# Performance work log

Measured on AMD Instinct MI355X. Metric: run time of the kernel, lower is better.

Reference implementation:

```python
import jax, jax.numpy as jnp
import numpy as np

KH, KW = 3, 3
SH, SW = 1, 1
IC, OC = 32, 32
M = 4
P = M * M
ITERS = 3
LAM = 1.0
EPS = 1e-8


def _patches(t, kh, kw, sh, sw):
    # t: [B, H, W, ...] -> [B, Ho, Wo, kh, kw, ...] (im2col, matches torch unfold+permute)
    H, W = t.shape[1], t.shape[2]
    Ho = (H - kh) // sh + 1
    Wo = (W - kw) // sw + 1
    i = (jnp.arange(Ho) * sh)[:, None] + jnp.arange(kh)[None, :]  # [Ho,kh]
    j = (jnp.arange(Wo) * sw)[:, None] + jnp.arange(kw)[None, :]  # [Wo,kw]
    tp = t[:, i]            # [B,Ho,kh,W,...]
    tp = tp[:, :, :, j]     # [B,Ho,kh,Wo,kw,...]
    return jnp.moveaxis(tp, 2, 3)  # [B,Ho,Wo,kh,kw,...]


def setup_inputs() -> dict:
    key = jax.random.key(0)
    k1, k2, k3, k4, k5 = jax.random.split(key, 5)
    x = jax.random.normal(k1, (4, 14, 14, IC, M, M), dtype=jnp.float32)
    a = jax.random.uniform(k2, (4, 14, 14, IC), dtype=jnp.float32)
    W = jax.random.uniform(k3, (KH, KW, IC, OC, M, M), dtype=jnp.float32)   # torch.rand init
    beta_u = jax.random.uniform(k4, (1, OC, 1), dtype=jnp.float32)
    beta_a = jax.random.uniform(k5, (1, OC), dtype=jnp.float32)
    return {"x": x, "a": a, "W": W, "beta_u": beta_u, "beta_a": beta_a}


def reference(x, a, W, beta_u, beta_a):
    # im2col patches
    xp = _patches(x, KH, KW, SH, SW)          # [B,Ho,Wo,kh,kw,IC,M,M]
    ap = _patches(a, KH, KW, SH, SW)          # [B,Ho,Wo,kh,kw,IC]
    # pose-transform votes: per (kh,kw,inCap,outCap) 4x4 matmul
    V = jnp.einsum('bhwklcxy,klcoyz->bhwklcoxz', xp, W)
    B, Ho, Wo = V.shape[:3]
    N = KH * KW * IC
    V = V.reshape(B, Ho, Wo, N, OC, P)        # votes
    a_in = ap.reshape(B, Ho, Wo, N)
    bu = beta_u.reshape(OC, 1)
    ba = beta_a.reshape(OC)

    # EM routing (Hinton et al. 2018, fixed inverse temperature)
    R = jnp.full((B, Ho, Wo, N, OC), 1.0 / OC, dtype=V.dtype)
    for it in range(ITERS):
        Ra = R * a_in[..., None]                                  # [B,Ho,Wo,N,OC]
        Rs = Ra.sum(axis=3) + EPS                                 # [B,Ho,Wo,OC]
        mu = jnp.einsum('bhwno,bhwnop->bhwop', Ra, V) / Rs[..., None]
        d = V - mu[:, :, :, None]                                 # [B,Ho,Wo,N,OC,P]
        sig2 = jnp.einsum('bhwno,bhwnop->bhwop', Ra, d * d) / Rs[..., None] + EPS
        cost = (bu + 0.5 * jnp.log(sig2)) * Rs[..., None]         # [B,Ho,Wo,OC,P]
        a_out = jax.nn.sigmoid(LAM * (ba - cost.sum(-1)))         # [B,Ho,Wo,OC]
        if it < ITERS - 1:
            logp = -0.5 * jnp.sum(d * d / sig2[:, :, :, None] + jnp.log(sig2)[:, :, :, None], axis=-1)
            R = jax.nn.softmax(jnp.log(a_out + EPS)[:, :, :, None] + logp, axis=-1)

    pose = mu.reshape(B, Ho, Wo, OC, M, M)
    return pose, a_out
```

## Files before the change

### kernel.cpp

```cpp
#include <hip/hip_runtime.h>


#define EPSV 1e-8f

template <int CTRL>
__device__ __forceinline__ float dppf(float v) {
  return __int_as_float(__builtin_amdgcn_update_dpp(
      0, __float_as_int(v), CTRL, 0xf, 0xf, true));
}
__device__ __forceinline__ float swz16(float v) {
  return __int_as_float(__builtin_amdgcn_ds_swizzle(__float_as_int(v), 0x401F));
}
__device__ __forceinline__ float red_max32(float v) {
  v = fmaxf(v, dppf<0xB1>(v));
  v = fmaxf(v, dppf<0x4E>(v));
  v = fmaxf(v, dppf<0x141>(v));
  v = fmaxf(v, dppf<0x140>(v));
  v = fmaxf(v, swz16(v));
  return v;
}
__device__ __forceinline__ float red_sum32(float v) {
  v += dppf<0xB1>(v);
  v += dppf<0x4E>(v);
  v += dppf<0x141>(v);
  v += dppf<0x140>(v);
  v += swz16(v);
  return v;
}

__device__ __forceinline__ void compute_votes(const float* __restrict__ Wt,
                                              const float* __restrict__ xr,
                                              int n, int o, float* __restrict__ V)
{
  float Wf[16];
  {
    const float* wp = Wt + (((n << 5) + o) << 4);
#pragma unroll
    for (int i = 0; i < 4; ++i) {
      const float4 q = *(const float4*)(wp + (i << 2));
      Wf[i*4+0]=q.x; Wf[i*4+1]=q.y; Wf[i*4+2]=q.z; Wf[i*4+3]=q.w;
    }
  }
  float xv[16];
#pragma unroll
  for (int i = 0; i < 4; ++i) {
    const float4 q = *(const float4*)(xr + (i << 2));
    xv[i*4+0]=q.x; xv[i*4+1]=q.y; xv[i*4+2]=q.z; xv[i*4+3]=q.w;
  }
#pragma unroll
  for (int xi = 0; xi < 4; ++xi)
#pragma unroll
    for (int z = 0; z < 4; ++z)
      V[xi*4+z] = fmaf(xv[xi*4+0], Wf[z],
                  fmaf(xv[xi*4+1], Wf[4+z],
                  fmaf(xv[xi*4+2], Wf[8+z],
                       xv[xi*4+3]* Wf[12+z])));
}

__global__ __launch_bounds__(512, 4) void caps_stats(
    const float* __restrict__ X, const float* __restrict__ A, const float* __restrict__ Wt,
    const float* __restrict__ Bu, const float* __restrict__ Ba,
    const float* __restrict__ prev, float* __restrict__ cur, int it)
{
  __shared__ float xp_s[144*16];
  __shared__ float a_s[144];
  __shared__ float part[8*544];
  __shared__ float prs[8*32];
  __shared__ float mu_t[512], isig_t[512], lsig_t[512];
  __shared__ float la_s[32], slog_s[32], rs_s[32];

  const int t    = threadIdx.x;
  const int o    = t & 31;
  const int ng   = t >> 5;
  const int wv   = t >> 6;
  const int lane = t & 63;

  const int bid  = blockIdx.x;
  const int pos  = bid >> 1;
  const int half = bid & 1;
  const int b  = pos / 144;
  const int r_ = pos - b*144;
  const int h  = r_ / 12;
  const int w  = r_ - (r_/12)*12;
  const int nbase = half * 144;

  for (int i = t; i < 576; i += 512) {
    const int r  = i >> 2, q4 = i & 3;
    const int n  = nbase + r;
    const int kl = n >> 5, c = n & 31;
    const int hy = h + kl/3, wx = w + (kl - (kl/3)*3);
    const float4 v = *(const float4*)(X + ((((b*14+hy)*14+wx) << 9) + (c << 4) + (q4 << 2)));
    *(float4*)(xp_s + (r << 4) + (q4 << 2)) = v;
  }
  if (t < 144) {
    const int n  = nbase + t;
    const int kl = n >> 5, c = n & 31;
    const int hy = h + kl/3, wx = w + (kl - (kl/3)*3);
    a_s[t] = A[((b*14+hy)*14+wx)*32 + c];
  }

  float mu_r[16], isig_r[16];
  float la_r = 0.f, slog_r = 0.f;

  if (it > 0) {
    {
      const int pi = t >> 5, oo = t & 31;
      const float* h0 = prev + (pos*2+0)*1056;
      const float* h1 = prev + (pos*2+1)*1056;
      const int idx = pi*32 + oo;
      const float s1   = h0[idx]       + h1[idx];
      const float s2   = h0[512+idx]   + h1[512+idx];
      const float rsum = h0[1024+oo]   + h1[1024+oo] + EPSV;
      const float mu = s1 / rsum;
      float var = s2 / rsum - mu*mu;
      var = fmaxf(var, 0.f);
      const float sg = var + EPSV;
      mu_t[idx]   = mu;
      isig_t[idx] = 1.0f / sg;
      lsig_t[idx] = __logf(sg);
      if (pi == 0) rs_s[oo] = rsum;
    }
    __syncthreads();
    if (t < 32) {
      float slog = 0.f;
#pragma unroll
      for (int p = 0; p < 16; ++p) slog += lsig_t[p*32 + t];
      const float cost = rs_s[t] * (16.0f*Bu[t] + 0.5f*slog);
      const float av = 1.0f / (1.0f + __expf(-(Ba[t] - cost)));
      la_s[t]   = __logf(av + EPSV);
      slog_s[t] = slog;
    }
    __syncthreads();
#pragma unroll
    for (int p = 0; p < 16; ++p) { mu_r[p] = mu_t[p*32 + o]; isig_r[p] = isig_t[p*32 + o]; }
    slog_r = slog_s[o];
    la_r   = la_s[o];
  } else {
#pragma unroll
    for (int p = 0; p < 16; ++p) { mu_r[p] = 0.f; isig_r[p] = 0.f; }
    __syncthreads();
  }

  float S1[16], S2[16];
#pragma unroll
  for (int p = 0; p < 16; ++p) { S1[p] = 0.f; S2[p] = 0.f; }
  float rs = 0.f;

#pragma unroll 1
  for (int j = 0; j < 9; ++j) {
    const int nl = ng + (j << 4);
    const int n  = nbase + nl;
    float V[16];
    compute_votes(Wt, xp_s + (nl << 4), n, o, V);

    float ra;
    if (it == 0) {
      ra = a_s[nl] * (1.0f/32.0f);
    } else {
      float q0 = 0.f, q1 = 0.f, q2 = 0.f, q3 = 0.f;
#pragma unroll
      for (int p = 0; p < 4; ++p) {
        float d;
        d = V[p]    - mu_r[p];    q0 = fmaf(d*d, isig_r[p],    q0);
        d = V[p+4]  - mu_r[p+4];  q1 = fmaf(d*d, isig_r[p+4],  q1);
        d = V[p+8]  - mu_r[p+8];  q2 = fmaf(d*d, isig_r[p+8],  q2);
        d = V[p+12] - mu_r[p+12]; q3 = fmaf(d*d, isig_r[p+12], q3);
      }
      const float q = slog_r + ((q0 + q1) + (q2 + q3));
      const float z = la_r - 0.5f*q;
      const float m  = red_max32(z);
      const float ev = __expf(z - m);
      const float s  = red_sum32(ev);
      ra = (ev / s) * a_s[nl];
    }
    rs += ra;
#pragma unroll
    for (int p = 0; p < 16; ++p) {
      const float rv = ra * V[p];
      S1[p] += rv;
      S2[p] = fmaf(rv, V[p], S2[p]);
    }
  }

#pragma unroll
  for (int p = 0; p < 16; ++p) {
    S1[p] += __shfl_xor(S1[p], 32);
    S2[p] += __shfl_xor(S2[p], 32);
  }
  rs += __shfl_xor(rs, 32);

  float* dst = cur + bid*1056;

  if (lane < 32) {
    float* p1 = part + wv*544 + o*17;
#pragma unroll
    for (int p = 0; p < 16; ++p) p1[p] = S1[p];
    prs[wv*32 + o] = rs;
  }
  __syncthreads();
  {
    const int pi = t >> 5, oo = t & 31;
    float s1 = 0.f;
#pragma unroll
    for (int g = 0; g < 8; ++g) s1 += part[g*544 + oo*17 + pi];
    dst[t] = s1;
    if (t < 32) {
      float r = 0.f;
#pragma unroll
      for (int g = 0; g < 8; ++g) r += prs[(g << 5) + t];
      dst[1024 + t] = r;
    }
  }
  __syncthreads();

  if (lane < 32) {
    float* p2 = part + wv*544 + o*17;
#pragma unroll
    for (int p = 0; p < 16; ++p) p2[p] = S2[p];
  }
  __syncthreads();
  {
    const int pi = t >> 5, oo = t & 31;
    float s2 = 0.f;
#pragma unroll
    for (int g = 0; g < 8; ++g) s2 += part[g*544 + oo*17 + pi];
    dst[512 + t] = s2;
  }
}

__global__ __launch_bounds__(512, 4) void caps_final(
    const float* __restrict__ prev, const float* __restrict__ Bu,
    const float* __restrict__ Ba, float* __restrict__ Out)
{
  __shared__ float mu_t[512], lsig_t[512], rs_s[32], aout_s[32];

  const int t   = threadIdx.x;
  const int pos = blockIdx.x;
  {
    const int pi = t >> 5, oo = t & 31;
    const float* h0 = prev + (pos*2+0)*1056;
    const float* h1 = prev + (pos*2+1)*1056;
    const int idx = pi*32 + oo;
    const float s1   = h0[idx]     + h1[idx];
    const float s2   = h0[512+idx] + h1[512+idx];
    const float rsum = h0[1024+oo] + h1[1024+oo] + EPSV;
    const float mu = s1 / rsum;
    float var = s2 / rsum - mu*mu;
    var = fmaxf(var, 0.f);
    mu_t[idx]   = mu;
    lsig_t[idx] = __logf(var + EPSV);
    if (pi == 0) rs_s[oo] = rsum;
  }
  __syncthreads();
  if (t < 32) {
    float slog = 0.f;
#pragma unroll
    for (int p = 0; p < 16; ++p) slog += lsig_t[p*32 + t];
    const float cost = rs_s[t] * (16.0f*Bu[t] + 0.5f*slog);
    aout_s[t] = 1.0f / (1.0f + __expf(-(Ba[t] - cost)));
  }
  __syncthreads();
  {
    const int oo = t >> 4, pi = t & 15;
    Out[pos*512 + t] = mu_t[pi*32 + oo];
  }
  if (t < 32) Out[294912 + pos*32 + t] = aout_s[t];
}

extern "C" void kernel_launch(void* const* d_in, const int* in_sizes, int n_in,
                              void* d_out, int out_size, void* d_ws, size_t ws_size,
                              hipStream_t stream) {
  (void)in_sizes; (void)n_in; (void)ws_size; (void)out_size;
  const float* X  = (const float*)d_in[0];
  const float* A  = (const float*)d_in[1];
  const float* Wt = (const float*)d_in[2];
  const float* Bu = (const float*)d_in[3];
  const float* Ba = (const float*)d_in[4];
  float* Out = (float*)d_out;

  float* pa = (float*)d_ws;
  float* pb = pa + 1152*1056;

  hipLaunchKernelGGL(caps_stats, dim3(1152), dim3(512), 0, stream,
                     X, A, Wt, Bu, Ba, (const float*)nullptr, pa, 0);
  hipLaunchKernelGGL(caps_stats, dim3(1152), dim3(512), 0, stream,
                     X, A, Wt, Bu, Ba, pa, pb, 1);
  hipLaunchKernelGGL(caps_stats, dim3(1152), dim3(512), 0, stream,
                     X, A, Wt, Bu, Ba, pb, pa, 2);
  hipLaunchKernelGGL(caps_final, dim3(576), dim3(512), 0, stream,
                     pa, Bu, Ba, Out);
}
```

Baseline: 164.9 us.

## Split input capsules into six chunks per position and add combine kernel

```diff
diff --git a/kernel.cpp b/kernel.cpp
--- a/kernel.cpp
+++ b/kernel.cpp
@@ -2,6 +2,11 @@
 
 
 #define EPSV 1e-8f
+#define NPOS 576
+#define NCHUNK 6
+#define CHN 48
+#define PSZ 1056
+#define SSZ 1088
 
 template <int CTRL>
 __device__ __forceinline__ float dppf(float v) {
@@ -58,16 +63,14 @@
 }
 
 __global__ __launch_bounds__(512, 4) void caps_stats(
-    const float* __restrict__ X, const float* __restrict__ A, const float* __restrict__ Wt,
-    const float* __restrict__ Bu, const float* __restrict__ Ba,
-    const float* __restrict__ prev, float* __restrict__ cur, int it)
+    const float* __restrict__ X, const float* __restrict__ A,
+    const float* __restrict__ Wt,
+    const float* __restrict__ Sb, float* __restrict__ P, int it)
 {
-  __shared__ float xp_s[144*16];
-  __shared__ float a_s[144];
+  __shared__ float xp_s[CHN*16];
+  __shared__ float a_s[CHN];
   __shared__ float part[8*544];
   __shared__ float prs[8*32];
-  __shared__ float mu_t[512], isig_t[512], lsig_t[512];
-  __shared__ float la_s[32], slog_s[32], rs_s[32];
 
   const int t    = threadIdx.x;
   const int o    = t & 31;
@@ -75,24 +78,24 @@
   const int wv   = t >> 6;
   const int lane = t & 63;
 
-  const int bid  = blockIdx.x;
-  const int pos  = bid >> 1;
-  const int half = bid & 1;
+  const int bid   = blockIdx.x;
+  const int chunk = bid / NPOS;
+  const int pos   = bid - chunk * NPOS;
   const int b  = pos / 144;
   const int r_ = pos - b*144;
   const int h  = r_ / 12;
   const int w  = r_ - (r_/12)*12;
-  const int nbase = half * 144;
-
-  for (int i = t; i < 576; i += 512) {
-    const int r  = i >> 2, q4 = i & 3;
+  const int nbase = chunk * CHN;
+
+  if (t < 192) {
+    const int r  = t >> 2, q4 = t & 3;
     const int n  = nbase + r;
     const int kl = n >> 5, c = n & 31;
     const int hy = h + kl/3, wx = w + (kl - (kl/3)*3);
     const float4 v = *(const float4*)(X + ((((b*14+hy)*14+wx) << 9) + (c << 4) + (q4 << 2)));
     *(float4*)(xp_s + (r << 4) + (q4 << 2)) = v;
   }
-  if (t < 144) {
+  if (t < CHN) {
     const int n  = nbase + t;
     const int kl = n >> 5, c = n & 31;
     const int hy = h + kl/3, wx = w + (kl - (kl/3)*3);
@@ -101,45 +104,20 @@
 
   float mu_r[16], isig_r[16];
   float la_r = 0.f, slog_r = 0.f;
-
   if (it > 0) {
-    {
-      const int pi = t >> 5, oo = t & 31;
-      const float* h0 = prev + (pos*2+0)*1056;
-      const float* h1 = prev + (pos*2+1)*1056;
-      const int idx = pi*32 + oo;
-      const float s1   = h0[idx]       + h1[idx];
-      const float s2   = h0[512+idx]   + h1[512+idx];
-      const float rsum = h0[1024+oo]   + h1[1024+oo] + EPSV;
-      const float mu = s1 / rsum;
-      float var = s2 / rsum - mu*mu;
-      var = fmaxf(var, 0.f);
-      const float sg = var + EPSV;
-      mu_t[idx]   = mu;
-      isig_t[idx] = 1.0f / sg;
-      lsig_t[idx] = __logf(sg);
-      if (pi == 0) rs_s[oo] = rsum;
-    }
-    __syncthreads();
-    if (t < 32) {
-      float slog = 0.f;
-#pragma unroll
-      for (int p = 0; p < 16; ++p) slog += lsig_t[p*32 + t];
-      const float cost = rs_s[t] * (16.0f*Bu[t] + 0.5f*slog);
-      const float av = 1.0f / (1.0f + __expf(-(Ba[t] - cost)));
-      la_s[t]   = __logf(av + EPSV);
-      slog_s[t] = slog;
-    }
-    __syncthreads();
-#pragma unroll
-    for (int p = 0; p < 16; ++p) { mu_r[p] = mu_t[p*32 + o]; isig_r[p] = isig_t[p*32 + o]; }
-    slog_r = slog_s[o];
-    la_r   = la_s[o];
+    const float* S = Sb + (size_t)pos * SSZ;
+#pragma unroll
+    for (int p = 0; p < 16; ++p) {
+      mu_r[p]   = S[p*32 + o];
+      isig_r[p] = S[512 + p*32 + o];
+    }
+    la_r   = S[1024 + o];
+    slog_r = S[1056 + o];
   } else {
 #pragma unroll
     for (int p = 0; p < 16; ++p) { mu_r[p] = 0.f; isig_r[p] = 0.f; }
-    __syncthreads();
-  }
+  }
+  __syncthreads();
 
   float S1[16], S2[16];
 #pragma unroll
@@ -147,7 +125,7 @@
   float rs = 0.f;
 
 #pragma unroll 1
-  for (int j = 0; j < 9; ++j) {
+  for (int j = 0; j < 3; ++j) {
     const int nl = ng + (j << 4);
     const int n  = nbase + nl;
     float V[16];
@@ -189,7 +167,7 @@
   }
   rs += __shfl_xor(rs, 32);
 
-  float* dst = cur + bid*1056;
+  float* dst = P + ((size_t)pos * NCHUNK + chunk) * PSZ;
 
   if (lane < 32) {
     float* p1 = part + wv*544 + o*17;
@@ -228,8 +206,50 @@
   }
 }
 
+__global__ __launch_bounds__(512, 4) void caps_combine(
+    const float* __restrict__ P, const float* __restrict__ Bu,
+    const float* __restrict__ Ba, float* __restrict__ Sb)
+{
+  __shared__ float lsig_t[512], rs_s[32];
+
+  const int t   = threadIdx.x;
+  const int o   = t & 31;
+  const int pos = blockIdx.x;
+  float* S = Sb + (size_t)pos * SSZ;
+  {
+    const float* hp = P + (size_t)pos * (NCHUNK * PSZ);
+    float s1 = 0.f, s2 = 0.f, rsum = 0.f;
+#pragma unroll
+    for (int cc = 0; cc < NCHUNK; ++cc) {
+      const float* hc = hp + cc * PSZ;
+      s1   += hc[t];
+      s2   += hc[512 + t];
+      rsum += hc[1024 + o];
+    }
+    rsum += EPSV;
+    const float mu = s1 / rsum;
+    float var = s2 / rsum - mu*mu;
+    var = fmaxf(var, 0.f);
+    const float sg = var + EPSV;
+    S[t]        = mu;
+    S[512 + t]  = 1.0f / sg;
+    lsig_t[t]   = __logf(sg);
+    if (t < 32) rs_s[t] = rsum;
+  }
+  __syncthreads();
+  if (t < 32) {
+    float slog = 0.f;
+#pragma unroll
+    for (int p = 0; p < 16; ++p) slog += lsig_t[p*32 + t];
+    const float cost = rs_s[t] * (16.0f*Bu[t] + 0.5f*slog);
+    const float av = 1.0f / (1.0f + __expf(-(Ba[t] - cost)));
+    S[1024 + t] = __logf(av + EPSV);
+    S[1056 + t] = slog;
+  }
+}
+
 __global__ __launch_bounds__(512, 4) void caps_final(
-    const float* __restrict__ prev, const float* __restrict__ Bu,
+    const float* __restrict__ P, const float* __restrict__ Bu,
     const float* __restrict__ Ba, float* __restrict__ Out)
 {
   __shared__ float mu_t[512], lsig_t[512], rs_s[32], aout_s[32];
@@ -237,19 +257,23 @@
   const int t   = threadIdx.x;
   const int pos = blockIdx.x;
   {
-    const int pi = t >> 5, oo = t & 31;
-    const float* h0 = prev + (pos*2+0)*1056;
-    const float* h1 = prev + (pos*2+1)*1056;
-    const int idx = pi*32 + oo;
-    const float s1   = h0[idx]     + h1[idx];
-    const float s2   = h0[512+idx] + h1[512+idx];
-    const float rsum = h0[1024+oo] + h1[1024+oo] + EPSV;
+    const int oo = t & 31;
+    const float* hp = P + (size_t)pos * (NCHUNK * PSZ);
+    float s1 = 0.f, s2 = 0.f, rsum = 0.f;
+#pragma unroll
+    for (int cc = 0; cc < NCHUNK; ++cc) {
+      const float* hc = hp + cc * PSZ;
+      s1   += hc[t];
+      s2   += hc[512 + t];
+      rsum += hc[1024 + oo];
+    }
+    rsum += EPSV;
     const float mu = s1 / rsum;
     float var = s2 / rsum - mu*mu;
     var = fmaxf(var, 0.f);
-    mu_t[idx]   = mu;
-    lsig_t[idx] = __logf(var + EPSV);
-    if (pi == 0) rs_s[oo] = rsum;
+    mu_t[t]   = mu;
+    lsig_t[t] = __logf(var + EPSV);
+    if (t < 32) rs_s[t] = rsum;
   }
   __syncthreads();
   if (t < 32) {
@@ -278,15 +302,19 @@
   const float* Ba = (const float*)d_in[4];
   float* Out = (float*)d_out;
 
-  float* pa = (float*)d_ws;
-  float* pb = pa + 1152*1056;
-
-  hipLaunchKernelGGL(caps_stats, dim3(1152), dim3(512), 0, stream,
-                     X, A, Wt, Bu, Ba, (const float*)nullptr, pa, 0);
-  hipLaunchKernelGGL(caps_stats, dim3(1152), dim3(512), 0, stream,
-                     X, A, Wt, Bu, Ba, pa, pb, 1);
-  hipLaunchKernelGGL(caps_stats, dim3(1152), dim3(512), 0, stream,
-                     X, A, Wt, Bu, Ba, pb, pa, 2);
-  hipLaunchKernelGGL(caps_final, dim3(576), dim3(512), 0, stream,
-                     pa, Bu, Ba, Out);
-}
+  float* P  = (float*)d_ws;
+  float* Sb = P + (size_t)NPOS * NCHUNK * PSZ;
+
+  hipLaunchKernelGGL(caps_stats, dim3(NPOS*NCHUNK), dim3(512), 0, stream,
+                     X, A, Wt, (const float*)nullptr, P, 0);
+  hipLaunchKernelGGL(caps_combine, dim3(NPOS), dim3(512), 0, stream,
+                     P, Bu, Ba, Sb);
+  hipLaunchKernelGGL(caps_stats, dim3(NPOS*NCHUNK), dim3(512), 0, stream,
+                     X, A, Wt, Sb, P, 1);
+  hipLaunchKernelGGL(caps_combine, dim3(NPOS), dim3(512), 0, stream,
+                     P, Bu, Ba, Sb);
+  hipLaunchKernelGGL(caps_stats, dim3(NPOS*NCHUNK), dim3(512), 0, stream,
+                     X, A, Wt, Sb, P, 2);
+  hipLaunchKernelGGL(caps_final, dim3(NPOS), dim3(512), 0, stream,
+                     P, Bu, Ba, Out);
+}
```

Measured after the change: 186.6 us. 1.13x slower.

## Fuse all EM routing iterations into one kernel with one block per position

Applied to the files above, without the earlier changes.

```diff
diff --git a/kernel.cpp b/kernel.cpp
--- a/kernel.cpp
+++ b/kernel.cpp
@@ -57,17 +57,17 @@
                        xv[xi*4+3]* Wf[12+z])));
 }
 
-__global__ __launch_bounds__(512, 4) void caps_stats(
-    const float* __restrict__ X, const float* __restrict__ A, const float* __restrict__ Wt,
-    const float* __restrict__ Bu, const float* __restrict__ Ba,
-    const float* __restrict__ prev, float* __restrict__ cur, int it)
+__global__ __launch_bounds__(512, 3) void caps_fused(
+    const float* __restrict__ X, const float* __restrict__ A,
+    const float* __restrict__ Wt, const float* __restrict__ Bu,
+    const float* __restrict__ Ba, float* __restrict__ Out)
 {
-  __shared__ float xp_s[144*16];
-  __shared__ float a_s[144];
+  __shared__ float xp_s[288*16];
+  __shared__ float a_s[288];
   __shared__ float part[8*544];
   __shared__ float prs[8*32];
   __shared__ float mu_t[512], isig_t[512], lsig_t[512];
-  __shared__ float la_s[32], slog_s[32], rs_s[32];
+  __shared__ float la_s[32], slog_s[32], rs_s[32], aout_s[32];
 
   const int t    = threadIdx.x;
   const int o    = t & 31;
@@ -75,50 +75,122 @@
   const int wv   = t >> 6;
   const int lane = t & 63;
 
-  const int bid  = blockIdx.x;
-  const int pos  = bid >> 1;
-  const int half = bid & 1;
+  const int pos = blockIdx.x;
   const int b  = pos / 144;
   const int r_ = pos - b*144;
   const int h  = r_ / 12;
   const int w  = r_ - (r_/12)*12;
-  const int nbase = half * 144;
-
-  for (int i = t; i < 576; i += 512) {
+
+  for (int i = t; i < 1152; i += 512) {
     const int r  = i >> 2, q4 = i & 3;
-    const int n  = nbase + r;
-    const int kl = n >> 5, c = n & 31;
+    const int kl = r >> 5, c = r & 31;
     const int hy = h + kl/3, wx = w + (kl - (kl/3)*3);
     const float4 v = *(const float4*)(X + ((((b*14+hy)*14+wx) << 9) + (c << 4) + (q4 << 2)));
     *(float4*)(xp_s + (r << 4) + (q4 << 2)) = v;
   }
-  if (t < 144) {
-    const int n  = nbase + t;
-    const int kl = n >> 5, c = n & 31;
+  if (t < 288) {
+    const int kl = t >> 5, c = t & 31;
     const int hy = h + kl/3, wx = w + (kl - (kl/3)*3);
     a_s[t] = A[((b*14+hy)*14+wx)*32 + c];
   }
+  __syncthreads();
 
   float mu_r[16], isig_r[16];
   float la_r = 0.f, slog_r = 0.f;
-
-  if (it > 0) {
+#pragma unroll
+  for (int p = 0; p < 16; ++p) { mu_r[p] = 0.f; isig_r[p] = 0.f; }
+
+#pragma unroll 1
+  for (int it = 0; it < 3; ++it) {
+    float S1[16], S2[16];
+#pragma unroll
+    for (int p = 0; p < 16; ++p) { S1[p] = 0.f; S2[p] = 0.f; }
+    float rs = 0.f;
+
+#pragma unroll 1
+    for (int j = 0; j < 18; ++j) {
+      const int nl = ng + (j << 4);
+      float V[16];
+      compute_votes(Wt, xp_s + (nl << 4), nl, o, V);
+
+      float ra;
+      if (it == 0) {
+        ra = a_s[nl] * (1.0f/32.0f);
+      } else {
+        float q0 = 0.f, q1 = 0.f, q2 = 0.f, q3 = 0.f;
+#pragma unroll
+        for (int p = 0; p < 4; ++p) {
+          float d;
+          d = V[p]    - mu_r[p];    q0 = fmaf(d*d, isig_r[p],    q0);
+          d = V[p+4]  - mu_r[p+4];  q1 = fmaf(d*d, isig_r[p+4],  q1);
+          d = V[p+8]  - mu_r[p+8];  q2 = fmaf(d*d, isig_r[p+8],  q2);
+          d = V[p+12] - mu_r[p+12]; q3 = fmaf(d*d, isig_r[p+12], q3);
+        }
+        const float q = slog_r + ((q0 + q1) + (q2 + q3));
+        const float z = la_r - 0.5f*q;
+        const float m  = red_max32(z);
+        const float ev = __expf(z - m);
+        const float s  = red_sum32(ev);
+        ra = (ev / s) * a_s[nl];
+      }
+      rs += ra;
+#pragma unroll
+      for (int p = 0; p < 16; ++p) {
+        const float rv = ra * V[p];
+        S1[p] += rv;
+        S2[p] = fmaf(rv, V[p], S2[p]);
+      }
+    }
+
+#pragma unroll
+    for (int p = 0; p < 16; ++p) {
+      S1[p] += __shfl_xor(S1[p], 32);
+      S2[p] += __shfl_xor(S2[p], 32);
+    }
+    rs += __shfl_xor(rs, 32);
+
+    if (lane < 32) {
+      float* p1 = part + wv*544 + o*17;
+#pragma unroll
+      for (int p = 0; p < 16; ++p) p1[p] = S1[p];
+      prs[wv*32 + o] = rs;
+    }
+    __syncthreads();
+    float s1v;
     {
       const int pi = t >> 5, oo = t & 31;
-      const float* h0 = prev + (pos*2+0)*1056;
-      const float* h1 = prev + (pos*2+1)*1056;
-      const int idx = pi*32 + oo;
-      const float s1   = h0[idx]       + h1[idx];
-      const float s2   = h0[512+idx]   + h1[512+idx];
-      const float rsum = h0[1024+oo]   + h1[1024+oo] + EPSV;
-      const float mu = s1 / rsum;
+      float s1 = 0.f;
+#pragma unroll
+      for (int g = 0; g < 8; ++g) s1 += part[g*544 + oo*17 + pi];
+      s1v = s1;
+      if (t < 32) {
+        float r = 0.f;
+#pragma unroll
+        for (int g = 0; g < 8; ++g) r += prs[(g << 5) + t];
+        rs_s[t] = r + EPSV;
+      }
+    }
+    __syncthreads();
+
+    if (lane < 32) {
+      float* p2 = part + wv*544 + o*17;
+#pragma unroll
+      for (int p = 0; p < 16; ++p) p2[p] = S2[p];
+    }
+    __syncthreads();
+    {
+      const int pi = t >> 5, oo = t & 31;
+      float s2 = 0.f;
+#pragma unroll
+      for (int g = 0; g < 8; ++g) s2 += part[g*544 + oo*17 + pi];
+      const float rsum = rs_s[oo];
+      const float mu = s1v / rsum;
       float var = s2 / rsum - mu*mu;
       var = fmaxf(var, 0.f);
       const float sg = var + EPSV;
-      mu_t[idx]   = mu;
-      isig_t[idx] = 1.0f / sg;
-      lsig_t[idx] = __logf(sg);
-      if (pi == 0) rs_s[oo] = rsum;
+      mu_t[t]   = mu;
+      isig_t[t] = 1.0f / sg;
+      lsig_t[t] = __logf(sg);
     }
     __syncthreads();
     if (t < 32) {
@@ -129,137 +201,17 @@
       const float av = 1.0f / (1.0f + __expf(-(Ba[t] - cost)));
       la_s[t]   = __logf(av + EPSV);
       slog_s[t] = slog;
-    }
-    __syncthreads();
-#pragma unroll
-    for (int p = 0; p < 16; ++p) { mu_r[p] = mu_t[p*32 + o]; isig_r[p] = isig_t[p*32 + o]; }
-    slog_r = slog_s[o];
-    la_r   = la_s[o];
-  } else {
-#pragma unroll
-    for (int p = 0; p < 16; ++p) { mu_r[p] = 0.f; isig_r[p] = 0.f; }
-    __syncthreads();
-  }
-
-  float S1[16], S2[16];
-#pragma unroll
-  for (int p = 0; p < 16; ++p) { S1[p] = 0.f; S2[p] = 0.f; }
-  float rs = 0.f;
-
-#pragma unroll 1
-  for (int j = 0; j < 9; ++j) {
-    const int nl = ng + (j << 4);
-    const int n  = nbase + nl;
-    float V[16];
-    compute_votes(Wt, xp_s + (nl << 4), n, o, V);
-
-    float ra;
-    if (it == 0) {
-      ra = a_s[nl] * (1.0f/32.0f);
-    } else {
-      float q0 = 0.f, q1 = 0.f, q2 = 0.f, q3 = 0.f;
-#pragma unroll
-      for (int p = 0; p < 4; ++p) {
-        float d;
-        d = V[p]    - mu_r[p];    q0 = fmaf(d*d, isig_r[p],    q0);
-        d = V[p+4]  - mu_r[p+4];  q1 = fmaf(d*d, isig_r[p+4],  q1);
-        d = V[p+8]  - mu_r[p+8];  q2 = fmaf(d*d, isig_r[p+8],  q2);
-        d = V[p+12] - mu_r[p+12]; q3 = fmaf(d*d, isig_r[p+12], q3);
-      }
-      const float q = slog_r + ((q0 + q1) + (q2 + q3));
-      const float z = la_r - 0.5f*q;
-      const float m  = red_max32(z);
-      const float ev = __expf(z - m);
-      const float s  = red_sum32(ev);
-      ra = (ev / s) * a_s[nl];
-    }
-    rs += ra;
-#pragma unroll
-    for (int p = 0; p < 16; ++p) {
-      const float rv = ra * V[p];
-      S1[p] += rv;
-      S2[p] = fmaf(rv, V[p], S2[p]);
-    }
-  }
-
-#pragma unroll
-  for (int p = 0; p < 16; ++p) {
-    S1[p] += __shfl_xor(S1[p], 32);
-    S2[p] += __shfl_xor(S2[p], 32);
-  }
-  rs += __shfl_xor(rs, 32);
-
-  float* dst = cur + bid*1056;
-
-  if (lane < 32) {
-    float* p1 = part + wv*544 + o*17;
-#pragma unroll
-    for (int p = 0; p < 16; ++p) p1[p] = S1[p];
-    prs[wv*32 + o] = rs;
-  }
-  __syncthreads();
-  {
-    const int pi = t >> 5, oo = t & 31;
-    float s1 = 0.f;
-#pragma unroll
-    for (int g = 0; g < 8; ++g) s1 += part[g*544 + oo*17 + pi];
-    dst[t] = s1;
-    if (t < 32) {
-      float r = 0.f;
-#pragma unroll
-      for (int g = 0; g < 8; ++g) r += prs[(g << 5) + t];
-      dst[1024 + t] = r;
-    }
-  }
-  __syncthreads();
-
-  if (lane < 32) {
-    float* p2 = part + wv*544 + o*17;
-#pragma unroll
-    for (int p = 0; p < 16; ++p) p2[p] = S2[p];
-  }
-  __syncthreads();
-  {
-    const int pi = t >> 5, oo = t & 31;
-    float s2 = 0.f;
-#pragma unroll
-    for (int g = 0; g < 8; ++g) s2 += part[g*544 + oo*17 + pi];
-    dst[512 + t] = s2;
-  }
-}
-
-__global__ __launch_bounds__(512, 4) void caps_final(
-    const float* __restrict__ prev, const float* __restrict__ Bu,
-    const float* __restrict__ Ba, float* __restrict__ Out)
-{
-  __shared__ float mu_t[512], lsig_t[512], rs_s[32], aout_s[32];
-
-  const int t   = threadIdx.x;
-  const int pos = blockIdx.x;
-  {
-    const int pi = t >> 5, oo = t & 31;
-    const float* h0 = prev + (pos*2+0)*1056;
-    const float* h1 = prev + (pos*2+1)*1056;
-    const int idx = pi*32 + oo;
-    const float s1   = h0[idx]     + h1[idx];
-    const float s2   = h0[512+idx] + h1[512+idx];
-    const float rsum = h0[1024+oo] + h1[1024+oo] + EPSV;
-    const float mu = s1 / rsum;
-    float var = s2 / rsum - mu*mu;
-    var = fmaxf(var, 0.f);
-    mu_t[idx]   = mu;
-    lsig_t[idx] = __logf(var + EPSV);
-    if (pi == 0) rs_s[oo] = rsum;
-  }
-  __syncthreads();
-  if (t < 32) {
-    float slog = 0.f;
-#pragma unroll
-    for (int p = 0; p < 16; ++p) slog += lsig_t[p*32 + t];
-    const float cost = rs_s[t] * (16.0f*Bu[t] + 0.5f*slog);
-    aout_s[t] = 1.0f / (1.0f + __expf(-(Ba[t] - cost)));
-  }
-  __syncthreads();
+      aout_s[t] = av;
+    }
+    __syncthreads();
+    if (it < 2) {
+#pragma unroll
+      for (int p = 0; p < 16; ++p) { mu_r[p] = mu_t[p*32 + o]; isig_r[p] = isig_t[p*32 + o]; }
+      slog_r = slog_s[o];
+      la_r   = la_s[o];
+    }
+  }
+
   {
     const int oo = t >> 4, pi = t & 15;
     Out[pos*512 + t] = mu_t[pi*32 + oo];
@@ -270,7 +222,7 @@
 extern "C" void kernel_launch(void* const* d_in, const int* in_sizes, int n_in,
                               void* d_out, int out_size, void* d_ws, size_t ws_size,
                               hipStream_t stream) {
-  (void)in_sizes; (void)n_in; (void)ws_size; (void)out_size;
+  (void)in_sizes; (void)n_in; (void)d_ws; (void)ws_size; (void)out_size;
   const float* X  = (const float*)d_in[0];
   const float* A  = (const float*)d_in[1];
   const float* Wt = (const float*)d_in[2];
@@ -278,15 +230,6 @@
   const float* Ba = (const float*)d_in[4];
   float* Out = (float*)d_out;
 
-  float* pa = (float*)d_ws;
-  float* pb = pa + 1152*1056;
-
-  hipLaunchKernelGGL(caps_stats, dim3(1152), dim3(512), 0, stream,
-                     X, A, Wt, Bu, Ba, (const float*)nullptr, pa, 0);
-  hipLaunchKernelGGL(caps_stats, dim3(1152), dim3(512), 0, stream,
-                     X, A, Wt, Bu, Ba, pa, pb, 1);
-  hipLaunchKernelGGL(caps_stats, dim3(1152), dim3(512), 0, stream,
-                     X, A, Wt, Bu, Ba, pb, pa, 2);
-  hipLaunchKernelGGL(caps_final, dim3(576), dim3(512), 0, stream,
-                     pa, Bu, Ba, Out);
-}
+  hipLaunchKernelGGL(caps_fused, dim3(576), dim3(512), 0, stream,
+                     X, A, Wt, Bu, Ba, Out);
+}
```

New measurement: 180.0 us. +9.1%, slower.
